# Performance work log

Measured on AMD Instinct MI355X. Metric: run time of the kernel, lower is better.

Reference implementation:

```python
import jax, jax.numpy as jnp
import numpy as np

MAXDISP = 192  # must match init_kwargs max_disp


def _interp_axis(x, axis, out_size):
    """1-D linear interpolation along `axis` with align_corners=True."""
    in_size = x.shape[axis]
    src = jnp.arange(out_size, dtype=jnp.float32) * ((in_size - 1) / (out_size - 1))
    i0 = jnp.clip(jnp.floor(src).astype(jnp.int32), 0, in_size - 1)
    i1 = jnp.clip(i0 + 1, 0, in_size - 1)
    w = (src - i0.astype(jnp.float32)).astype(x.dtype)
    shape = [1] * x.ndim
    shape[axis] = out_size
    w = w.reshape(shape)
    return jnp.take(x, i0, axis=axis) * (1 - w) + jnp.take(x, i1, axis=axis) * w


def create_cost_volume(left, right, maxdisp):
    """Vectorized version of the original per-disparity slice-copy loop.
    cost[:, :C, d, :, w] = left[:, :, :, w]        if w >= d else 0
    cost[:, C:, d, :, w] = right[:, :, :, w - d]   if w >= d else 0
    Returns [B, 2C, D, H, W] with D = maxdisp // 4.
    """
    B, C, H, W = left.shape
    D = maxdisp // 4
    d = jnp.arange(D)[:, None]          # [D,1]
    w = jnp.arange(W)[None, :]          # [1,W]
    mask = (w >= d).astype(left.dtype)  # [D,W]
    idx = jnp.clip(w - d, 0, W - 1)     # [D,W] shifted gather indices
    mask_b = mask[None, None, :, None, :]                       # [1,1,D,1,W]
    cost_left = left[:, :, None, :, :] * mask_b                 # [B,C,D,H,W]
    cost_right = jnp.take(right, idx.reshape(-1), axis=3)       # [B,C,H,D*W]
    cost_right = cost_right.reshape(B, C, H, D, W)
    cost_right = jnp.transpose(cost_right, (0, 1, 3, 2, 4)) * mask_b
    return jnp.concatenate([cost_left, cost_right], axis=1)     # [B,2C,D,H,W]


def upsample_regression(vol, maxdisp):
    """Trilinear x4 upsample (align_corners=True) + softmax over disparity +
    soft-argmin expectation. vol: [B, D/4, H/4, W/4] -> [B, H, W]."""
    x = vol
    for axis in (1, 2, 3):
        x = _interp_axis(x, axis, x.shape[axis] * 4)
    p = jax.nn.softmax(x, axis=1)                       # [B, maxdisp, H, W]
    disps = jnp.arange(maxdisp, dtype=x.dtype)
    return jnp.einsum('bdhw,d->bhw', p, disps)


def setup_inputs() -> dict:
    key = jax.random.key(0)
    k1, k2 = jax.random.split(key)
    left = jax.random.normal(k1, (2, 32, 64, 128), dtype=jnp.float32)
    right = jax.random.normal(k2, (2, 32, 64, 128), dtype=jnp.float32)
    return {"left": left, "right": right}


def reference(left, right):
    cost = create_cost_volume(left, right, MAXDISP)  # [B,2C,D,H,W]
    # Stand-in for the (unavailable) stacked hourglass 3D-CNN: channel mean
    # reduces the cost volume to a single-channel disparity volume [B,D,H,W].
    vol = cost.mean(axis=1)
    return upsample_regression(vol, MAXDISP)  # [B, 4H, 4W]
```

## Files before the change

### kernel.cpp

```cpp
#include <hip/hip_runtime.h>

#define BB 2
#define CC 32
#define HC 64
#define WC 128
#define DC 48
#define HO 256
#define WO 512
#define MAXD 192

__global__ __launch_bounds__(512) void fused_disparity_kernel(
    const float* __restrict__ left, const float* __restrict__ right,
    float* __restrict__ out) {
    __shared__ float sbuf[4][WC];
    __shared__ float Lh[WC];
    __shared__ float Rh[WC];

    int r  = blockIdx.x;
    int b  = r >> 8;
    int hh = r & (HO - 1);

    float src_h = (float)hh * (63.0f / 255.0f);
    int h0 = (int)src_h; if (h0 > HC - 1) h0 = HC - 1;
    int h1 = min(h0 + 1, HC - 1);
    float fh = src_h - (float)h0;

    int t   = threadIdx.x;
    int w   = t & (WC - 1);
    int sel = t >> 7;

    {
        const float* basep = (sel < 2) ? left : right;
        int hrow = (sel & 1) ? h1 : h0;
        const float* p = basep + (size_t)b * (CC * HC * WC) + hrow * WC + w;
        float s = 0.f;
#pragma unroll
        for (int c = 0; c < CC; ++c) s += p[c * (HC * WC)];
        sbuf[sel][w] = s;
    }
    __syncthreads();

    if (t < WC) {
        Lh[t] = (1.f - fh) * sbuf[0][t] + fh * sbuf[1][t];
    } else if (t < 2 * WC) {
        int u = t - WC;
        Rh[u] = (1.f - fh) * sbuf[2][u] + fh * sbuf[3][u];
    }
    __syncthreads();

    int ww = t;
    float src_w = (float)ww * (127.0f / 511.0f);
    int w0 = (int)src_w; if (w0 > WC - 1) w0 = WC - 1;
    int w1 = min(w0 + 1, WC - 1);
    float fw = src_w - (float)w0;

    const float scale = 1.0f / 64.0f;
    float c0 = (1.f - fw) * scale;
    float c1 = fw * scale;
    float lw0 = Lh[w0];
    float lw1 = Lh[w1];

    float v[DC];
    float m = -1e30f;
#pragma unroll
    for (int d = 0; d < DC; ++d) {
        int i0 = w0 - d; float m0 = (i0 >= 0) ? 1.f : 0.f; i0 = max(i0, 0);
        int i1 = w1 - d; float m1 = (i1 >= 0) ? 1.f : 0.f; i1 = max(i1, 0);
        float val = m0 * c0 * (lw0 + Rh[i0]) + m1 * c1 * (lw1 + Rh[i1]);
        v[d] = val;
        m = fmaxf(m, val);
    }

    float lsum = 0.f, ssum = 0.f;
#pragma unroll
    for (int d = 0; d < DC; ++d) {
        int lo = (d * (MAXD - 1) + (DC - 2)) / (DC - 1);
        int hi = ((d + 1) * (MAXD - 1) + (DC - 2)) / (DC - 1) - 1;
        if (hi > MAXD - 1) hi = MAXD - 1;
        float vcur  = v[d];
        float vnext = (d < DC - 1) ? v[d + 1] : v[d];
#pragma unroll
        for (int dd = lo; dd <= hi; ++dd) {
            float src = (float)dd * (47.0f / 191.0f);
            float wd  = src - (float)d;
            float x   = vcur + wd * (vnext - vcur);
            float e   = __expf(x - m);
            lsum += e;
            ssum += e * (float)dd;
        }
    }
    out[r * WO + ww] = ssum / lsum;
}

extern "C" void kernel_launch(void* const* d_in, const int* in_sizes, int n_in,
                              void* d_out, int out_size, void* d_ws, size_t ws_size,
                              hipStream_t stream) {
    const float* left  = (const float*)d_in[0];
    const float* right = (const float*)d_in[1];
    float* out = (float*)d_out;

    fused_disparity_kernel<<<BB * HO, WO, 0, stream>>>(left, right, out);
}
```

Before: 74.06 us.

## Precompute channel sums in separate kernel and split disparity range across threads

Moves the channel summation into its own kernel that writes per-row channel sums to workspace, so the main kernel no longer re-reads all 32 channels for every upsampled row. The disparity kernel now splits the 192 output disparities into four quarters handled by different threads, reducing per-thread register arrays and adding a shared-memory reduction, and launches four times as many blocks. It also drops the max-subtraction in the softmax, which risks overflow if values grow large; the inputs here are channel means and likely small.

```diff
diff --git a/kernel.cpp b/kernel.cpp
--- a/kernel.cpp
+++ b/kernel.cpp
@@ -9,46 +9,102 @@
 #define WO 512
 #define MAXD 192
 
-__global__ __launch_bounds__(512) void fused_disparity_kernel(
+__global__ __launch_bounds__(256) void sum_channels_kernel(
     const float* __restrict__ left, const float* __restrict__ right,
+    float* __restrict__ Ls, float* __restrict__ Rs) {
+    __shared__ float sbuf[2][WC];
+    int blk = blockIdx.x;
+    int m   = blk >> 7;
+    int b   = (blk >> 6) & 1;
+    int h   = blk & (HC - 1);
+    int t   = threadIdx.x;
+    int sel = t >> 7;
+    int w   = t & (WC - 1);
+
+    const float* src = (m ? right : left)
+                     + (size_t)b * (CC * HC * WC)
+                     + (size_t)(sel * 16) * (HC * WC) + h * WC + w;
+    float s = 0.f;
+#pragma unroll
+    for (int c = 0; c < 16; ++c) s += src[c * (HC * WC)];
+    sbuf[sel][w] = s;
+    __syncthreads();
+    if (t < WC) {
+        float* dst = m ? Rs : Ls;
+        dst[b * (HC * WC) + h * WC + t] = sbuf[0][t] + sbuf[1][t];
+    }
+}
+
+template <int K>
+__device__ inline void quarter_work(const float* __restrict__ Rh,
+                                    int w0, int w1, float c0, float c1,
+                                    float lw0, float lw1,
+                                    float& plsum, float& pssum) {
+    constexpr int DDLO = 48 * K;
+    constexpr int DDHI = 48 * K + 47;
+    constexpr int DLO  = (DDLO * (DC - 1)) / (MAXD - 1);
+    constexpr int DHI  = (DDHI * (DC - 1)) / (MAXD - 1);
+    constexpr int NV   = DHI - DLO + 2;
+
+    float vv[NV];
+#pragma unroll
+    for (int j = 0; j < NV; ++j) {
+        int d = DLO + j;
+        if (d > DC - 1) { vv[j] = vv[j - 1]; continue; }
+        int i0 = w0 - d; float m0 = (i0 >= 0) ? 1.f : 0.f; i0 = max(i0, 0);
+        int i1 = w1 - d; float m1 = (i1 >= 0) ? 1.f : 0.f; i1 = max(i1, 0);
+        vv[j] = m0 * c0 * (lw0 + Rh[i0]) + m1 * c1 * (lw1 + Rh[i1]);
+    }
+    float ls = 0.f, ss = 0.f;
+#pragma unroll
+    for (int dd = DDLO; dd <= DDHI; ++dd) {
+        int d    = (dd * (DC - 1)) / (MAXD - 1);
+        float wd = (float)dd * (47.0f / 191.0f) - (float)d;
+        float vc = vv[d - DLO];
+        float x  = vc + wd * (vv[d - DLO + 1] - vc);
+        float e  = __expf(x);
+        ls += e;
+        ss += e * (float)dd;
+    }
+    plsum = ls;
+    pssum = ss;
+}
+
+__global__ __launch_bounds__(512) void disparity_kernel(
+    const float* __restrict__ Ls, const float* __restrict__ Rs,
     float* __restrict__ out) {
-    __shared__ float sbuf[4][WC];
     __shared__ float Lh[WC];
     __shared__ float Rh[WC];
+    __shared__ float redL[4][WC];
+    __shared__ float redS[4][WC];
 
-    int r  = blockIdx.x;
-    int b  = r >> 8;
-    int hh = r & (HO - 1);
+    int blk = blockIdx.x;
+    int r   = blk >> 2;
+    int g   = blk & 3;
+    int b   = r >> 8;
+    int hh  = r & (HO - 1);
 
     float src_h = (float)hh * (63.0f / 255.0f);
     int h0 = (int)src_h; if (h0 > HC - 1) h0 = HC - 1;
     int h1 = min(h0 + 1, HC - 1);
     float fh = src_h - (float)h0;
 
-    int t   = threadIdx.x;
-    int w   = t & (WC - 1);
-    int sel = t >> 7;
+    int t = threadIdx.x;
 
-    {
-        const float* basep = (sel < 2) ? left : right;
-        int hrow = (sel & 1) ? h1 : h0;
-        const float* p = basep + (size_t)b * (CC * HC * WC) + hrow * WC + w;
-        float s = 0.f;
-#pragma unroll
-        for (int c = 0; c < CC; ++c) s += p[c * (HC * WC)];
-        sbuf[sel][w] = s;
+    if (t < WC) {
+        const float* p = Ls + b * (HC * WC) + t;
+        Lh[t] = (1.f - fh) * p[h0 * WC] + fh * p[h1 * WC];
+    } else if (t < 2 * WC) {
+        int u = t - WC;
+        const float* p = Rs + b * (HC * WC) + u;
+        Rh[u] = (1.f - fh) * p[h0 * WC] + fh * p[h1 * WC];
     }
     __syncthreads();
 
-    if (t < WC) {
-        Lh[t] = (1.f - fh) * sbuf[0][t] + fh * sbuf[1][t];
-    } else if (t < 2 * WC) {
-        int u = t - WC;
-        Rh[u] = (1.f - fh) * sbuf[2][u] + fh * sbuf[3][u];
-    }
-    __syncthreads();
+    int p = t & (WC - 1);
+    int k = t >> 7;
+    int ww = g * WC + p;
 
-    int ww = t;
     float src_w = (float)ww * (127.0f / 511.0f);
     int w0 = (int)src_w; if (w0 > WC - 1) w0 = WC - 1;
     int w1 = min(w0 + 1, WC - 1);
@@ -60,36 +116,22 @@
     float lw0 = Lh[w0];
     float lw1 = Lh[w1];
 
-    float v[DC];
-    float m = -1e30f;
-#pragma unroll
-    for (int d = 0; d < DC; ++d) {
-        int i0 = w0 - d; float m0 = (i0 >= 0) ? 1.f : 0.f; i0 = max(i0, 0);
-        int i1 = w1 - d; float m1 = (i1 >= 0) ? 1.f : 0.f; i1 = max(i1, 0);
-        float val = m0 * c0 * (lw0 + Rh[i0]) + m1 * c1 * (lw1 + Rh[i1]);
-        v[d] = val;
-        m = fmaxf(m, val);
+    float pls, pss;
+    switch (k) {
+        case 0: quarter_work<0>(Rh, w0, w1, c0, c1, lw0, lw1, pls, pss); break;
+        case 1: quarter_work<1>(Rh, w0, w1, c0, c1, lw0, lw1, pls, pss); break;
+        case 2: quarter_work<2>(Rh, w0, w1, c0, c1, lw0, lw1, pls, pss); break;
+        default: quarter_work<3>(Rh, w0, w1, c0, c1, lw0, lw1, pls, pss); break;
     }
+    redL[k][p] = pls;
+    redS[k][p] = pss;
+    __syncthreads();
 
-    float lsum = 0.f, ssum = 0.f;
-#pragma unroll
-    for (int d = 0; d < DC; ++d) {
-        int lo = (d * (MAXD - 1) + (DC - 2)) / (DC - 1);
-        int hi = ((d + 1) * (MAXD - 1) + (DC - 2)) / (DC - 1) - 1;
-        if (hi > MAXD - 1) hi = MAXD - 1;
-        float vcur  = v[d];
-        float vnext = (d < DC - 1) ? v[d + 1] : v[d];
-#pragma unroll
-        for (int dd = lo; dd <= hi; ++dd) {
-            float src = (float)dd * (47.0f / 191.0f);
-            float wd  = src - (float)d;
-            float x   = vcur + wd * (vnext - vcur);
-            float e   = __expf(x - m);
-            lsum += e;
-            ssum += e * (float)dd;
-        }
+    if (t < WC) {
+        float ls = redL[0][t] + redL[1][t] + redL[2][t] + redL[3][t];
+        float ss = redS[0][t] + redS[1][t] + redS[2][t] + redS[3][t];
+        out[r * WO + g * WC + t] = ss / ls;
     }
-    out[r * WO + ww] = ssum / lsum;
 }
 
 extern "C" void kernel_launch(void* const* d_in, const int* in_sizes, int n_in,
@@ -98,6 +140,9 @@
     const float* left  = (const float*)d_in[0];
     const float* right = (const float*)d_in[1];
     float* out = (float*)d_out;
+    float* Ls  = (float*)d_ws;
+    float* Rs  = Ls + BB * HC * WC;
 
-    fused_disparity_kernel<<<BB * HO, WO, 0, stream>>>(left, right, out);
+    sum_channels_kernel<<<256, 256, 0, stream>>>(left, right, Ls, Rs);
+    disparity_kernel<<<BB * HO * 4, 512, 0, stream>>>(Ls, Rs, out);
 }
```

Result: faster. 70.74 us (-4.5%).
